# Kernel optimization log

Measured on AMD Instinct MI355X. Metric: run time of the kernel, lower is better.

The kernel has to match this reference:

```python
import jax, jax.numpy as jnp
import numpy as np

N_NODES = 100000
N_EDGES = 1600000
N_FEAT = 256
HIDDEN = 128


def setup_inputs() -> dict:
    key = jax.random.key(0)
    k1, k2, k3, k4 = jax.random.split(key, 4)
    x = jax.random.normal(k1, (N_NODES, N_FEAT), dtype=jnp.float32)
    edge_index = jax.random.randint(k2, (2, N_EDGES), 0, N_NODES, dtype=jnp.int64)
    # GCNConv linear weight (PyG Linear: out = x @ W.T), bias added after aggregation
    W = jax.random.normal(k3, (HIDDEN, N_FEAT), dtype=jnp.float32) / np.sqrt(N_FEAT)
    b = jnp.zeros((HIDDEN,), dtype=jnp.float32)
    # PReLU per-channel slope, torch default init 0.25
    prelu_a = jnp.full((HIDDEN,), 0.25, dtype=jnp.float32)
    return {"x": x, "edge_index": edge_index, "W": W, "b": b, "prelu_a": prelu_a}


def reference(x, edge_index, W, b, prelu_a):
    N = x.shape[0]
    # dense linear transform first (as PyG GCNConv does)
    h = x @ W.T  # [N, hidden]
    # add self-loops
    loops = jnp.arange(N, dtype=edge_index.dtype)
    row = jnp.concatenate([edge_index[0], loops])  # source
    col = jnp.concatenate([edge_index[1], loops])  # target
    # symmetric normalization: deg computed over target index (PyG gcn_norm)
    ones = jnp.ones(row.shape[0], dtype=h.dtype)
    deg = jax.ops.segment_sum(ones, col, num_segments=N)
    dinv = jnp.where(deg > 0, jax.lax.rsqrt(deg), 0.0)
    norm = dinv[row] * dinv[col]  # [E+N]
    # gather source features, scale, scatter-sum to targets
    msg = h[row] * norm[:, None]  # [E+N, hidden]
    agg = jax.ops.segment_sum(msg, col, num_segments=N) + b  # [N, hidden]
    # PReLU with per-channel slope
    return jnp.where(agg > 0, agg, prelu_a * agg)
```

## Files before the change

### kernel.cpp

```cpp
#include <hip/hip_runtime.h>
#include <hip/hip_fp16.h>
#include <stdint.h>

#define N_NODES 100000
#define N_EDGES 1600000
#define N_FEAT 256
#define HIDDEN 128
#define SCAN_CHUNK 1024
#define NB ((N_NODES + SCAN_CHUNK - 1) / SCAN_CHUNK)

#define BKT_SH 8
#define BKT_RANGE 256
#define NBKT ((N_NODES + BKT_RANGE - 1) >> BKT_SH)
#define BKT_CAP 4608
#define BIN_CHUNK 4096
#define NWG_BIN ((N_EDGES + BIN_CHUNK - 1) / BIN_CHUNK)

typedef __attribute__((ext_vector_type(8))) short bf16x8;
typedef __attribute__((ext_vector_type(4))) float f32x4;


__global__ __launch_bounds__(256) void k_zerog(int* __restrict__ g) {
    int i = blockIdx.x * 256 + threadIdx.x;
    if (i < NBKT) g[i] = 0;
}


__global__ __launch_bounds__(256) void k_bin(const int* __restrict__ row,
                                             const int* __restrict__ col,
                                             int* __restrict__ gcur,
                                             int2* __restrict__ recs) {
    __shared__ int hcnt[NBKT];
    __shared__ int hbase[NBKT];
    const int t = threadIdx.x;
    for (int i = t; i < NBKT; i += 256) hcnt[i] = 0;
    __syncthreads();
    const int e0 = blockIdx.x * BIN_CHUNK;
    int cs[16], ss[16];
#pragma unroll
    for (int i = 0; i < 16; ++i) {
        int e = e0 + t + i * 256;
        if (e < N_EDGES) {
            cs[i] = col[e];
            ss[i] = row[e];
            atomicAdd(&hcnt[cs[i] >> BKT_SH], 1);
        } else {
            cs[i] = -1;
        }
    }
    __syncthreads();
    for (int i = t; i < NBKT; i += 256) {
        int c = hcnt[i];
        hbase[i] = (c > 0) ? atomicAdd(&gcur[i], c) : 0;
    }
    __syncthreads();
    for (int i = t; i < NBKT; i += 256) hcnt[i] = 0;
    __syncthreads();
#pragma unroll
    for (int i = 0; i < 16; ++i) {
        if (cs[i] >= 0) {
            int bkt = cs[i] >> BKT_SH;
            int pos = hbase[bkt] + atomicAdd(&hcnt[bkt], 1);
            if (pos < BKT_CAP)
                recs[(size_t)bkt * BKT_CAP + pos] = make_int2(cs[i], ss[i]);
        }
    }
}


__global__ __launch_bounds__(256) void k_hist(const int* __restrict__ gcur,
                                              const int2* __restrict__ recs,
                                              int* __restrict__ cnt,
                                              float* __restrict__ dinv) {
    __shared__ int hc[BKT_RANGE];
    const int b = blockIdx.x, t = threadIdx.x;
    hc[t] = 0;
    __syncthreads();
    int n = gcur[b];
    if (n > BKT_CAP) n = BKT_CAP;
    const int2* rb = recs + (size_t)b * BKT_CAP;
    for (int i = t; i < n; i += 256)
        atomicAdd(&hc[rb[i].x & (BKT_RANGE - 1)], 1);
    __syncthreads();
    int node = (b << BKT_SH) + t;
    if (node < N_NODES) {
        cnt[node] = hc[t];
        dinv[node] = rsqrtf((float)(hc[t] + 1));
    }
}


__global__ __launch_bounds__(256) void k_scan1(const int* __restrict__ cnt,
                                               int* __restrict__ row_ptr,
                                               int* __restrict__ bsum) {
    __shared__ int ts[256];
    int t = threadIdx.x;
    int base = blockIdx.x * SCAN_CHUNK + t * 4;
    int v[4];
#pragma unroll
    for (int i = 0; i < 4; ++i) { int idx = base + i; v[i] = (idx < N_NODES) ? cnt[idx] : 0; }
    int s = v[0] + v[1] + v[2] + v[3];
    int val = s;
    ts[t] = val;
    __syncthreads();
    for (int off = 1; off < 256; off <<= 1) {
        int other = (t >= off) ? ts[t - off] : 0;
        __syncthreads();
        val += other;
        ts[t] = val;
        __syncthreads();
    }
    int run = val - s;
#pragma unroll
    for (int i = 0; i < 4; ++i) {
        int idx = base + i;
        if (idx < N_NODES) row_ptr[idx] = run;
        run += v[i];
    }
    if (t == 255) bsum[blockIdx.x] = val;
}

__global__ void k_scan2(int* __restrict__ bsum, int* __restrict__ row_ptr) {
    if (threadIdx.x == 0) {
        int run = 0;
        for (int i = 0; i < NB; ++i) { int v = bsum[i]; bsum[i] = run; run += v; }
        row_ptr[N_NODES] = run;
    }
}

__global__ __launch_bounds__(256) void k_scan3(int* __restrict__ row_ptr,
                                               const int* __restrict__ bsum) {
    int t = threadIdx.x;
    int base = blockIdx.x * SCAN_CHUNK + t * 4;
    int add = bsum[blockIdx.x];
#pragma unroll
    for (int i = 0; i < 4; ++i) {
        int idx = base + i;
        if (idx < N_NODES) row_ptr[idx] += add;
    }
}


__global__ __launch_bounds__(256) void k_slot2(const int* __restrict__ gcur,
                                               const int2* __restrict__ recs,
                                               const int* __restrict__ row_ptr,
                                               int* __restrict__ edge_src) {
    __shared__ int cur[BKT_RANGE];
    __shared__ int rp[BKT_RANGE];
    const int b = blockIdx.x, t = threadIdx.x;
    cur[t] = 0;
    int node = (b << BKT_SH) + t;
    rp[t] = (node < N_NODES) ? row_ptr[node] : 0;
    __syncthreads();
    int n = gcur[b];
    if (n > BKT_CAP) n = BKT_CAP;
    const int2* rb = recs + (size_t)b * BKT_CAP;
    for (int i = t; i < n; i += 256) {
        int2 r = rb[i];
        int l = r.x & (BKT_RANGE - 1);
        int pos = rp[l] + atomicAdd(&cur[l], 1);
        edge_src[pos] = r.y;
    }
}


__global__ __launch_bounds__(256) void k_wconv(const float* __restrict__ W,
                                               short* __restrict__ w_hi,
                                               short* __restrict__ w_lo) {
    int i = blockIdx.x * 256 + threadIdx.x;
    if (i < HIDDEN * N_FEAT) {
        float f = W[i];
        unsigned u = __float_as_uint(f);
        unsigned hb = u & 0xFFFF0000u;
        float r = f - __uint_as_float(hb);
        w_hi[i] = (short)(u >> 16);
        w_lo[i] = (short)(__float_as_uint(r) >> 16);
    }
}

#define TM 64
#define KS 32
#define LDR 40

__global__ __launch_bounds__(256) void k_gemm(const float* __restrict__ x,
                                              const short* __restrict__ w_hi,
                                              const short* __restrict__ w_lo,
                                              const float* __restrict__ dinv,
                                              __half* __restrict__ h2) {
    __shared__ short xh[TM * LDR];
    __shared__ short xl[TM * LDR];
    __shared__ short wh[HIDDEN * LDR];
    __shared__ short wl[HIDDEN * LDR];
    const int t = threadIdx.x;
    const int lane = t & 63;
    const int wv = t >> 6;
    const int wr = wv >> 1, wc = wv & 1;
    const int row0 = blockIdx.x * TM;

    f32x4 acc[2][4];
#pragma unroll
    for (int m = 0; m < 2; ++m)
#pragma unroll
        for (int n = 0; n < 4; ++n) acc[m][n] = (f32x4)0.f;

    const int rx = t >> 2, sx = t & 3;
    const int gxr = row0 + rx;
    const bool xok = (gxr < N_NODES);
    const int rw0 = t >> 2, rw1 = (t >> 2) + 64, slw = t & 3;

    for (int k0 = 0; k0 < N_FEAT; k0 += KS) {
        float4 f[2];
#pragma unroll
        for (int q = 0; q < 2; ++q) {
            f[q] = make_float4(0.f, 0.f, 0.f, 0.f);
            if (xok) f[q] = *(const float4*)&x[(size_t)gxr * N_FEAT + k0 + sx * 8 + q * 4];
        }
        unsigned hp[4], lp[4];
#pragma unroll
        for (int q = 0; q < 2; ++q) {
            float e0 = f[q].x, e1 = f[q].y, e2 = f[q].z, e3 = f[q].w;
            unsigned u0 = __float_as_uint(e0), u1 = __float_as_uint(e1);
            unsigned u2 = __float_as_uint(e2), u3 = __float_as_uint(e3);
            unsigned c0 = u0 & 0xFFFF0000u, c1 = u1 & 0xFFFF0000u;
            unsigned c2 = u2 & 0xFFFF0000u, c3 = u3 & 0xFFFF0000u;
            hp[q * 2 + 0] = (u0 >> 16) | c1;
            hp[q * 2 + 1] = (u2 >> 16) | c3;
            float r0 = e0 - __uint_as_float(c0), r1 = e1 - __uint_as_float(c1);
            float r2 = e2 - __uint_as_float(c2), r3 = e3 - __uint_as_float(c3);
            lp[q * 2 + 0] = (__float_as_uint(r0) >> 16) | (__float_as_uint(r1) & 0xFFFF0000u);
            lp[q * 2 + 1] = (__float_as_uint(r2) >> 16) | (__float_as_uint(r3) & 0xFFFF0000u);
        }
        {
            int o = rx * LDR + sx * 8;
            *(int4*)&xh[o] = make_int4(hp[0], hp[1], hp[2], hp[3]);
            *(int4*)&xl[o] = make_int4(lp[0], lp[1], lp[2], lp[3]);
        }
        {
            int4 a0 = *(const int4*)&w_hi[(size_t)rw0 * N_FEAT + k0 + slw * 8];
            int4 b0 = *(const int4*)&w_lo[(size_t)rw0 * N_FEAT + k0 + slw * 8];
            int4 a1 = *(const int4*)&w_hi[(size_t)rw1 * N_FEAT + k0 + slw * 8];
            int4 b1 = *(const int4*)&w_lo[(size_t)rw1 * N_FEAT + k0 + slw * 8];
            *(int4*)&wh[rw0 * LDR + slw * 8] = a0;
            *(int4*)&wl[rw0 * LDR + slw * 8] = b0;
            *(int4*)&wh[rw1 * LDR + slw * 8] = a1;
            *(int4*)&wl[rw1 * LDR + slw * 8] = b1;
        }
        __syncthreads();
        const int fr = lane & 15, fs = lane >> 4;
        bf16x8 ah[2], al[2], bh[4], bl[4];
#pragma unroll
        for (int m = 0; m < 2; ++m) {
            int o = (wr * 32 + m * 16 + fr) * LDR + fs * 8;
            ah[m] = *(const bf16x8*)&xh[o];
            al[m] = *(const bf16x8*)&xl[o];
        }
#pragma unroll
        for (int n = 0; n < 4; ++n) {
            int o = (wc * 64 + n * 16 + fr) * LDR + fs * 8;
            bh[n] = *(const bf16x8*)&wh[o];
            bl[n] = *(const bf16x8*)&wl[o];
        }
#pragma unroll
        for (int m = 0; m < 2; ++m)
#pragma unroll
            for (int n = 0; n < 4; ++n) {
                acc[m][n] = __builtin_amdgcn_mfma_f32_16x16x32_bf16(ah[m], bh[n], acc[m][n], 0, 0, 0);
                acc[m][n] = __builtin_amdgcn_mfma_f32_16x16x32_bf16(al[m], bh[n], acc[m][n], 0, 0, 0);
                acc[m][n] = __builtin_amdgcn_mfma_f32_16x16x32_bf16(ah[m], bl[n], acc[m][n], 0, 0, 0);
            }
        __syncthreads();
    }
    const int cr = (lane >> 4) * 4, cc = lane & 15;
#pragma unroll
    for (int m = 0; m < 2; ++m) {
        int gr0 = row0 + wr * 32 + m * 16 + cr;
#pragma unroll
        for (int r = 0; r < 4; ++r) {
            int gr = gr0 + r;
            if (gr < N_NODES) {
                float d = dinv[gr];
#pragma unroll
                for (int n = 0; n < 4; ++n) {
                    int gc = wc * 64 + n * 16 + cc;
                    h2[(size_t)gr * HIDDEN + gc] = __float2half_rn(acc[m][n][r] * d);
                }
            }
        }
    }
}


__global__ __launch_bounds__(256) void k_gather(const int* __restrict__ row_ptr,
                                                const int* __restrict__ edge_src,
                                                const float* __restrict__ dinv,
                                                const __half* __restrict__ h2s,
                                                const float* __restrict__ b,
                                                const float* __restrict__ pa,
                                                float* __restrict__ out) {
    int n = (blockIdx.x * 256 + threadIdx.x) >> 6;
    int lane = threadIdx.x & 63;
    if (n >= N_NODES) return;
    int start = row_ptr[n], end = row_ptr[n + 1];
    float dn = dinv[n];
    const __half2* hp = (const __half2*)h2s;
    float2 base = __half22float2(hp[(unsigned)n * 64u + lane]);
    float2 acc = make_float2(0.f, 0.f);
    for (int e = start; e < end; e += 16) {
        int idx[16];
        float wt[16];
#pragma unroll
        for (int i = 0; i < 16; ++i) {
            int ee = e + i;
            int cl = (ee < end) ? ee : (end - 1);
            idx[i] = edge_src[cl];
            wt[i] = (ee < end) ? 1.f : 0.f;
        }
        __half2 v[16];
#pragma unroll
        for (int i = 0; i < 16; ++i) v[i] = hp[(unsigned)idx[i] * 64u + lane];
#pragma unroll
        for (int i = 0; i < 16; ++i) {
            float2 f = __half22float2(v[i]);
            acc.x += f.x * wt[i];
            acc.y += f.y * wt[i];
        }
    }
    float2 bb = *(const float2*)&b[lane * 2];
    float2 aa = *(const float2*)&pa[lane * 2];
    float2 r;
    r.x = dn * (base.x + acc.x) + bb.x;
    r.y = dn * (base.y + acc.y) + bb.y;
    r.x = r.x > 0.f ? r.x : r.x * aa.x;
    r.y = r.y > 0.f ? r.y : r.y * aa.y;
    *(float2*)&out[(size_t)n * HIDDEN + lane * 2] = r;
}


extern "C" void kernel_launch(void* const* d_in, const int* in_sizes, int n_in,
                              void* d_out, int out_size, void* d_ws, size_t ws_size,
                              hipStream_t stream) {
    const float* x  = (const float*)d_in[0];
    const int*   ei = (const int*)d_in[1];
    const float* W  = (const float*)d_in[2];
    const float* b  = (const float*)d_in[3];
    const float* pa = (const float*)d_in[4];
    float* out = (float*)d_out;

    const int* row = ei;
    const int* col = ei + N_EDGES;

    char* w = (char*)d_ws;
    __half* h2      = (__half*)w;
    int*   cnt      = (int*)(w + (size_t)(N_NODES + 1) * HIDDEN * 2);
    int*   row_ptr  = cnt + N_NODES;
    int*   bsum     = row_ptr + (N_NODES + 2);
    int*   edge_src = bsum + 128;
    float* dinv     = (float*)(edge_src + N_EDGES);
    short* w_hi     = (short*)(dinv + N_NODES);
    short* w_lo     = w_hi + HIDDEN * N_FEAT;
    int*   gcur     = (int*)(w_lo + HIDDEN * N_FEAT);
    int2*  recs     = (int2*)(((uintptr_t)(gcur + NBKT) + 15) & ~(uintptr_t)15);

    k_zerog<<<(NBKT + 255) / 256, 256, 0, stream>>>(gcur);
    k_bin<<<NWG_BIN, 256, 0, stream>>>(row, col, gcur, recs);
    k_hist<<<NBKT, 256, 0, stream>>>(gcur, recs, cnt, dinv);
    k_scan1<<<NB, 256, 0, stream>>>(cnt, row_ptr, bsum);
    k_scan2<<<1, 64, 0, stream>>>(bsum, row_ptr);
    k_scan3<<<NB, 256, 0, stream>>>(row_ptr, bsum);
    k_slot2<<<NBKT, 256, 0, stream>>>(gcur, recs, row_ptr, edge_src);
    k_wconv<<<(HIDDEN * N_FEAT + 255) / 256, 256, 0, stream>>>(W, w_hi, w_lo);
    k_gemm<<<(N_NODES + TM - 1) / TM, 256, 0, stream>>>(x, w_hi, w_lo, dinv, h2);
    k_gather<<<(int)(((size_t)N_NODES * 64 + 255) / 256), 256, 0, stream>>>(
        row_ptr, edge_src, dinv, h2, b, pa, out);
}
```

Before: 165.8 us.

## Load GEMM MFMA operands directly from global memory, dropping LDS staging

The GEMM kernel no longer stages x and W tiles through shared memory with barriers. Each lane now loads its MFMA fragment straight from global memory, doing the bf16 hi/lo split in registers, and the K loop is not unrolled. This removes LDS writes and reads and the two __syncthreads per K step. In exchange, x rows are read redundantly by the two column-waves and W fragments by every block, so loads are less coalesced (32-byte segments per lane) and rely more on cache.

New measurement: 205.7 us. 1.24x slower.

```diff
diff --git a/kernel.cpp b/kernel.cpp
--- a/kernel.cpp
+++ b/kernel.cpp
@@ -179,23 +179,18 @@
 }
 
 #define TM 64
-#define KS 32
-#define LDR 40
 
 __global__ __launch_bounds__(256) void k_gemm(const float* __restrict__ x,
                                               const short* __restrict__ w_hi,
                                               const short* __restrict__ w_lo,
                                               const float* __restrict__ dinv,
                                               __half* __restrict__ h2) {
-    __shared__ short xh[TM * LDR];
-    __shared__ short xl[TM * LDR];
-    __shared__ short wh[HIDDEN * LDR];
-    __shared__ short wl[HIDDEN * LDR];
     const int t = threadIdx.x;
     const int lane = t & 63;
     const int wv = t >> 6;
     const int wr = wv >> 1, wc = wv & 1;
     const int row0 = blockIdx.x * TM;
+    const int fr = lane & 15, fs = lane >> 4;
 
     f32x4 acc[2][4];
 #pragma unroll
@@ -203,62 +198,57 @@
 #pragma unroll
         for (int n = 0; n < 4; ++n) acc[m][n] = (f32x4)0.f;
 
-    const int rx = t >> 2, sx = t & 3;
-    const int gxr = row0 + rx;
-    const bool xok = (gxr < N_NODES);
-    const int rw0 = t >> 2, rw1 = (t >> 2) + 64, slw = t & 3;
-
-    for (int k0 = 0; k0 < N_FEAT; k0 += KS) {
-        float4 f[2];
-#pragma unroll
-        for (int q = 0; q < 2; ++q) {
-            f[q] = make_float4(0.f, 0.f, 0.f, 0.f);
-            if (xok) f[q] = *(const float4*)&x[(size_t)gxr * N_FEAT + k0 + sx * 8 + q * 4];
-        }
-        unsigned hp[4], lp[4];
-#pragma unroll
-        for (int q = 0; q < 2; ++q) {
-            float e0 = f[q].x, e1 = f[q].y, e2 = f[q].z, e3 = f[q].w;
-            unsigned u0 = __float_as_uint(e0), u1 = __float_as_uint(e1);
-            unsigned u2 = __float_as_uint(e2), u3 = __float_as_uint(e3);
-            unsigned c0 = u0 & 0xFFFF0000u, c1 = u1 & 0xFFFF0000u;
-            unsigned c2 = u2 & 0xFFFF0000u, c3 = u3 & 0xFFFF0000u;
-            hp[q * 2 + 0] = (u0 >> 16) | c1;
-            hp[q * 2 + 1] = (u2 >> 16) | c3;
-            float r0 = e0 - __uint_as_float(c0), r1 = e1 - __uint_as_float(c1);
-            float r2 = e2 - __uint_as_float(c2), r3 = e3 - __uint_as_float(c3);
-            lp[q * 2 + 0] = (__float_as_uint(r0) >> 16) | (__float_as_uint(r1) & 0xFFFF0000u);
-            lp[q * 2 + 1] = (__float_as_uint(r2) >> 16) | (__float_as_uint(r3) & 0xFFFF0000u);
-        }
-        {
-            int o = rx * LDR + sx * 8;
-            *(int4*)&xh[o] = make_int4(hp[0], hp[1], hp[2], hp[3]);
-            *(int4*)&xl[o] = make_int4(lp[0], lp[1], lp[2], lp[3]);
-        }
-        {
-            int4 a0 = *(const int4*)&w_hi[(size_t)rw0 * N_FEAT + k0 + slw * 8];
-            int4 b0 = *(const int4*)&w_lo[(size_t)rw0 * N_FEAT + k0 + slw * 8];
-            int4 a1 = *(const int4*)&w_hi[(size_t)rw1 * N_FEAT + k0 + slw * 8];
-            int4 b1 = *(const int4*)&w_lo[(size_t)rw1 * N_FEAT + k0 + slw * 8];
-            *(int4*)&wh[rw0 * LDR + slw * 8] = a0;
-            *(int4*)&wl[rw0 * LDR + slw * 8] = b0;
-            *(int4*)&wh[rw1 * LDR + slw * 8] = a1;
-            *(int4*)&wl[rw1 * LDR + slw * 8] = b1;
-        }
-        __syncthreads();
-        const int fr = lane & 15, fs = lane >> 4;
-        bf16x8 ah[2], al[2], bh[4], bl[4];
+    int ar0 = row0 + wr * 32 + fr;
+    int ar1 = ar0 + 16;
+    const bool aok0 = (ar0 < N_NODES), aok1 = (ar1 < N_NODES);
+    const float* xp0 = &x[(size_t)(aok0 ? ar0 : 0) * N_FEAT + fs * 8];
+    const float* xp1 = &x[(size_t)(aok1 ? ar1 : 0) * N_FEAT + fs * 8];
+    const short* bp[4];
+    const short* cp[4];
+#pragma unroll
+    for (int n = 0; n < 4; ++n) {
+        int br = wc * 64 + n * 16 + fr;
+        bp[n] = &w_hi[(size_t)br * N_FEAT + fs * 8];
+        cp[n] = &w_lo[(size_t)br * N_FEAT + fs * 8];
+    }
+
+#pragma unroll 1
+    for (int k0 = 0; k0 < N_FEAT; k0 += 32) {
+        bf16x8 ah[2], al[2];
 #pragma unroll
         for (int m = 0; m < 2; ++m) {
-            int o = (wr * 32 + m * 16 + fr) * LDR + fs * 8;
-            ah[m] = *(const bf16x8*)&xh[o];
-            al[m] = *(const bf16x8*)&xl[o];
-        }
+            const float* xp = m ? xp1 : xp0;
+            const bool ok = m ? aok1 : aok0;
+            float4 g0 = make_float4(0.f, 0.f, 0.f, 0.f);
+            float4 g1 = make_float4(0.f, 0.f, 0.f, 0.f);
+            if (ok) {
+                g0 = *(const float4*)(xp + k0);
+                g1 = *(const float4*)(xp + k0 + 4);
+            }
+            float e[8] = {g0.x, g0.y, g0.z, g0.w, g1.x, g1.y, g1.z, g1.w};
+            unsigned hp[4], lp[4];
+#pragma unroll
+            for (int q = 0; q < 4; ++q) {
+                unsigned u0 = __float_as_uint(e[2 * q]);
+                unsigned u1 = __float_as_uint(e[2 * q + 1]);
+                unsigned c0 = u0 & 0xFFFF0000u, c1 = u1 & 0xFFFF0000u;
+                hp[q] = (u0 >> 16) | c1;
+                float r0 = e[2 * q] - __uint_as_float(c0);
+                float r1 = e[2 * q + 1] - __uint_as_float(c1);
+                lp[q] = (__float_as_uint(r0) >> 16) | (__float_as_uint(r1) & 0xFFFF0000u);
+            }
+            int4 hv = make_int4(hp[0], hp[1], hp[2], hp[3]);
+            int4 lv = make_int4(lp[0], lp[1], lp[2], lp[3]);
+            ah[m] = *(const bf16x8*)&hv;
+            al[m] = *(const bf16x8*)&lv;
+        }
+        bf16x8 bh[4], bl[4];
 #pragma unroll
         for (int n = 0; n < 4; ++n) {
-            int o = (wc * 64 + n * 16 + fr) * LDR + fs * 8;
-            bh[n] = *(const bf16x8*)&wh[o];
-            bl[n] = *(const bf16x8*)&wl[o];
+            int4 hv = *(const int4*)(bp[n] + k0);
+            int4 lv = *(const int4*)(cp[n] + k0);
+            bh[n] = *(const bf16x8*)&hv;
+            bl[n] = *(const bf16x8*)&lv;
         }
 #pragma unroll
         for (int m = 0; m < 2; ++m)
@@ -268,7 +258,6 @@
                 acc[m][n] = __builtin_amdgcn_mfma_f32_16x16x32_bf16(al[m], bh[n], acc[m][n], 0, 0, 0);
                 acc[m][n] = __builtin_amdgcn_mfma_f32_16x16x32_bf16(ah[m], bl[n], acc[m][n], 0, 0, 0);
             }
-        __syncthreads();
     }
     const int cr = (lane >> 4) * 4, cc = lane & 15;
 #pragma unroll
```
